# Performance work log

Hardware: AMD Instinct MI355X
Metric: run time of the kernel (lower is better)

Reference implementation:

```python
import jax, jax.numpy as jnp
import numpy as np

MASK_VALUE = -1e6  # torch code uses -1000000.0, not -inf


def setup_inputs() -> dict:
    key = jax.random.key(0)
    k1, k2, k3, k4 = jax.random.split(key, 4)
    B, Nq, Nk, d = 32, 2048, 2048, 128
    return {
        "querys": jax.random.normal(k1, (B, Nq, d), dtype=jnp.float32),
        "keys": jax.random.normal(k2, (B, Nk, d), dtype=jnp.float32),
        "values": jax.random.normal(k3, (B, Nk, d), dtype=jnp.float32),
        "valid_seq_len": jax.random.randint(k4, (B,), 1, Nk + 1, dtype=jnp.int32),
    }


def reference(querys, keys, values, valid_seq_len):
    # querys: [B, Nq, d], keys/values: [B, Nk, d], valid_seq_len: [B]
    d = querys.shape[-1]
    scale = 1.0 / jnp.sqrt(jnp.asarray(d, dtype=querys.dtype))
    # scores: [B, Nq, Nk]
    scores = jnp.einsum("bqd,bkd->bqk", querys, keys) * scale
    Nk = keys.shape[1]
    # mask key positions >= valid length (per batch, broadcast over queries)
    mask = jnp.arange(Nk, dtype=jnp.int32)[None, None, :] < valid_seq_len[:, None, None]
    scores = jnp.where(mask, scores, jnp.asarray(MASK_VALUE, dtype=scores.dtype))
    attn = jax.nn.softmax(scores, axis=-1)
    # dropout prob = 0.0 -> identity
    out = jnp.einsum("bqk,bkd->bqd", attn, values)
    return out
```

## Files before the change

kernel.cpp:

```cpp
#include <hip/hip_runtime.h>
#include <cstdint>
#include <math.h>

typedef unsigned short ushort_t;
typedef unsigned int uint_t;
typedef __bf16 v8bf __attribute__((ext_vector_type(8)));
typedef float v16f __attribute__((ext_vector_type(16)));

constexpr int B_SZ = 32, NQ = 2048, NK = 2048, DH = 128;
constexpr int BQ2 = 128, BK = 64;
constexpr int NQT = NQ / BQ2;
constexpr float QSCALE = 0.12751880226116815f;
constexpr float M2 = 17.312340490667561f;

__device__ inline int swzK(int row, int chunk) {
  return row * 128 + ((chunk ^ (row & 7)) << 3);
}
__device__ inline int swzV(int d, int chunk) {
  return d * 64 + ((chunk ^ (d & 7)) << 3);
}

__device__ __forceinline__ float4 ld4f(const float* p) {
  return *reinterpret_cast<const float4*>(p);
}
__device__ __forceinline__ uint4 ld4u(const ushort_t* p) {
  return *reinterpret_cast<const uint4*>(p);
}

__device__ inline v8bf cvt8(const float* __restrict__ p) {
  float4 f0 = ld4f(p);
  float4 f1 = ld4f(p + 4);
  v8bf r;
  r[0] = (__bf16)f0.x; r[1] = (__bf16)f0.y; r[2] = (__bf16)f0.z; r[3] = (__bf16)f0.w;
  r[4] = (__bf16)f1.x; r[5] = (__bf16)f1.y; r[6] = (__bf16)f1.z; r[7] = (__bf16)f1.w;
  return r;
}

__device__ inline v8bf cvt8s(const float* __restrict__ p, float s) {
  float4 f0 = ld4f(p);
  float4 f1 = ld4f(p + 4);
  v8bf r;
  r[0] = (__bf16)(f0.x * s); r[1] = (__bf16)(f0.y * s);
  r[2] = (__bf16)(f0.z * s); r[3] = (__bf16)(f0.w * s);
  r[4] = (__bf16)(f1.x * s); r[5] = (__bf16)(f1.y * s);
  r[6] = (__bf16)(f1.z * s); r[7] = (__bf16)(f1.w * s);
  return r;
}

__device__ inline v8bf cvt8r(const float4 f0, const float4 f1) {
  v8bf r;
  r[0] = (__bf16)f0.x; r[1] = (__bf16)f0.y; r[2] = (__bf16)f0.z; r[3] = (__bf16)f0.w;
  r[4] = (__bf16)f1.x; r[5] = (__bf16)f1.y; r[6] = (__bf16)f1.z; r[7] = (__bf16)f1.w;
  return r;
}

__device__ __forceinline__ uint_t pk2(float a, float b) {
  const ushort_t ua = __builtin_bit_cast(ushort_t, (__bf16)a);
  const ushort_t ub = __builtin_bit_cast(ushort_t, (__bf16)b);
  return (uint_t)ua | ((uint_t)ub << 16);
}

__global__ __launch_bounds__(256) void transpose_v(const float* __restrict__ V,
                                                   ushort_t* __restrict__ Vt) {
  __shared__ __align__(16) ushort_t st[64 * 128];
  const int b = blockIdx.y, k0 = blockIdx.x * 64, t = threadIdx.x;
  for (int c = 0; c < 4; ++c) {
    const int row = (t >> 4) + 16 * c;
    const int col = (t & 15) * 8;
    v8bf v = cvt8(V + ((size_t)(b * NK + k0 + row)) * DH + col);
    const int chunk = (col >> 3) ^ ((row >> 3) & 7);
    *reinterpret_cast<v8bf*>(&st[row * 128 + chunk * 8]) = v;
  }
  __syncthreads();
  for (int c = 0; c < 4; ++c) {
    const int d = (t >> 3) + 32 * c;
    const int kc = (t & 7) * 8;
    alignas(16) ushort_t tmp[8];
    for (int j = 0; j < 8; ++j) {
      const int row = kc + j;
      const int elem = (d & 7) | (((d >> 3) ^ ((row >> 3) & 7)) << 3);
      tmp[j] = st[row * 128 + elem];
    }
    *reinterpret_cast<uint4*>(Vt + ((size_t)(b * DH + d)) * NK + k0 + kc) =
        *reinterpret_cast<const uint4*>(tmp);
  }
}

__device__ __forceinline__ void qk_sm(const ushort_t* sk, int l32, int hi, int k0n,
                                      int valid, const v8bf* qf, float& ls0,
                                      float& ls1, uint4& pa0, uint4& pa1,
                                      uint4& pa2, uint4& pa3) {
  const bool part = (k0n + BK > valid);
#pragma unroll
  for (int kb = 0; kb < 2; ++kb) {
    const int rowA = kb * 32 + l32;
    const uint4 kf0 = ld4u(&sk[swzK(rowA, 0 + hi)]);
    const uint4 kf1 = ld4u(&sk[swzK(rowA, 2 + hi)]);
    const uint4 kf2 = ld4u(&sk[swzK(rowA, 4 + hi)]);
    const uint4 kf3 = ld4u(&sk[swzK(rowA, 6 + hi)]);
    const uint4 kf4 = ld4u(&sk[swzK(rowA, 8 + hi)]);
    const uint4 kf5 = ld4u(&sk[swzK(rowA, 10 + hi)]);
    const uint4 kf6 = ld4u(&sk[swzK(rowA, 12 + hi)]);
    const uint4 kf7 = ld4u(&sk[swzK(rowA, 14 + hi)]);
    v16f sa;
#pragma unroll
    for (int r = 0; r < 16; ++r) sa[r] = 0.f;
    __builtin_amdgcn_s_setprio(1);
    sa = __builtin_amdgcn_mfma_f32_32x32x16_bf16(__builtin_bit_cast(v8bf, kf0), qf[0], sa, 0, 0, 0);
    sa = __builtin_amdgcn_mfma_f32_32x32x16_bf16(__builtin_bit_cast(v8bf, kf1), qf[1], sa, 0, 0, 0);
    sa = __builtin_amdgcn_mfma_f32_32x32x16_bf16(__builtin_bit_cast(v8bf, kf2), qf[2], sa, 0, 0, 0);
    sa = __builtin_amdgcn_mfma_f32_32x32x16_bf16(__builtin_bit_cast(v8bf, kf3), qf[3], sa, 0, 0, 0);
    sa = __builtin_amdgcn_mfma_f32_32x32x16_bf16(__builtin_bit_cast(v8bf, kf4), qf[4], sa, 0, 0, 0);
    sa = __builtin_amdgcn_mfma_f32_32x32x16_bf16(__builtin_bit_cast(v8bf, kf5), qf[5], sa, 0, 0, 0);
    sa = __builtin_amdgcn_mfma_f32_32x32x16_bf16(__builtin_bit_cast(v8bf, kf6), qf[6], sa, 0, 0, 0);
    sa = __builtin_amdgcn_mfma_f32_32x32x16_bf16(__builtin_bit_cast(v8bf, kf7), qf[7], sa, 0, 0, 0);
    __builtin_amdgcn_s_setprio(0);
    float p[16];
#pragma unroll
    for (int r = 0; r < 16; ++r) {
      const int crow = (r & 3) + 8 * (r >> 2) + 4 * hi;
      float x = sa[r];
      if (part) x = (k0n + kb * 32 + crow < valid) ? x : -1e30f;
      float e;
      asm("v_exp_f32 %0, %1" : "=v"(e) : "v"(x - M2));
      p[r] = e;
      if (r < 8) ls0 += e; else ls1 += e;
    }
#pragma unroll
    for (int q2 = 0; q2 < 2; ++q2) {
      uint_t A0 = pk2(p[8 * q2 + 0], p[8 * q2 + 1]);
      uint_t A1 = pk2(p[8 * q2 + 2], p[8 * q2 + 3]);
      uint_t B0 = pk2(p[8 * q2 + 4], p[8 * q2 + 5]);
      uint_t B1 = pk2(p[8 * q2 + 6], p[8 * q2 + 7]);
      asm("v_permlane32_swap_b32 %0, %1" : "+v"(A0), "+v"(B0));
      asm("v_permlane32_swap_b32 %0, %1" : "+v"(A1), "+v"(B1));
      uint4 fw;
      fw.x = A0; fw.y = A1; fw.z = B0; fw.w = B1;
      if (kb == 0) { if (q2 == 0) pa0 = fw; else pa1 = fw; }
      else         { if (q2 == 0) pa2 = fw; else pa3 = fw; }
    }
  }
}

__device__ __forceinline__ void pv4(const ushort_t* sv, int l32, int hi,
                                    const uint4 paf, int ksg, v16f* o) {
  const uint4 vf0 = ld4u(&sv[swzV(0 + l32, 2 * ksg + hi)]);
  const uint4 vf1 = ld4u(&sv[swzV(32 + l32, 2 * ksg + hi)]);
  const uint4 vf2 = ld4u(&sv[swzV(64 + l32, 2 * ksg + hi)]);
  const uint4 vf3 = ld4u(&sv[swzV(96 + l32, 2 * ksg + hi)]);
  const v8bf pa = __builtin_bit_cast(v8bf, paf);
  __builtin_amdgcn_s_setprio(1);
  o[0] = __builtin_amdgcn_mfma_f32_32x32x16_bf16(pa, __builtin_bit_cast(v8bf, vf0), o[0], 0, 0, 0);
  o[1] = __builtin_amdgcn_mfma_f32_32x32x16_bf16(pa, __builtin_bit_cast(v8bf, vf1), o[1], 0, 0, 0);
  o[2] = __builtin_amdgcn_mfma_f32_32x32x16_bf16(pa, __builtin_bit_cast(v8bf, vf2), o[2], 0, 0, 0);
  o[3] = __builtin_amdgcn_mfma_f32_32x32x16_bf16(pa, __builtin_bit_cast(v8bf, vf3), o[3], 0, 0, 0);
  __builtin_amdgcn_s_setprio(0);
}

__global__ __launch_bounds__(256, 2) void attn(const float* __restrict__ Q,
                                               const float* __restrict__ K,
                                               const ushort_t* __restrict__ Vt,
                                               const int* __restrict__ vsl,
                                               float* __restrict__ Out) {
  __shared__ __align__(16) ushort_t sK2[2][64 * 128];
  __shared__ __align__(16) ushort_t sV2[2][DH * 64];

  const int t = threadIdx.x;
  const int lane = t & 63, w = t >> 6, hi = lane >> 5, l32 = lane & 31;

  int* s_ord = reinterpret_cast<int*>(sK2);
  if (t < 32) {
    const int cx = (vsl[t] + 63) >> 6;
    int rank = 0;
    for (int y = 0; y < 32; ++y) {
      const int cy = (vsl[y] + 63) >> 6;
      rank += (cy > cx) || (cy == cx && y < t);
    }
    s_ord[rank] = t;
  }
  __syncthreads();
  const int n = (int)blockIdx.x;
  const int ci = n & 255, cj = n >> 8;
  const int ru = cj ? 511 - ci : ci;
  const int b = s_ord[ru >> 4];
  const int qt2 = ru & 15;
  __syncthreads();

  const int q0 = qt2 * BQ2;
  const int valid = vsl[b];
  const int nt = (valid + BK - 1) / BK;

  v8bf qf[8];
  {
    const float* qp = Q + ((size_t)(b * NQ + q0 + w * 32 + l32)) * DH + hi * 8;
#pragma unroll
    for (int ks = 0; ks < 8; ++ks) qf[ks] = cvt8s(qp + ks * 16, QSCALE);
  }

  v16f o[4];
#pragma unroll
  for (int nb = 0; nb < 4; ++nb)
#pragma unroll
    for (int r = 0; r < 16; ++r) o[nb][r] = 0.f;
  float ls0 = 0.f, ls1 = 0.f;

  const float* Kb = K + (size_t)b * NK * DH;
  const ushort_t* Vb = Vt + (size_t)b * DH * NK;
  const int krow = t >> 4, kch = t & 15;
  const int vd = t >> 3, vch = t & 7;

  float4 k0a, k0b, k1a, k1b, k2a, k2b, k3a, k3b;
  uint4 v0r, v1r, v2r, v3r;

#define PREFETCH(KOFF)                                                   \
  do {                                                                   \
    const float* p0_ = Kb + (size_t)((KOFF) + krow) * DH + kch * 8;      \
    const float* p1_ = Kb + (size_t)((KOFF) + krow + 16) * DH + kch * 8; \
    const float* p2_ = Kb + (size_t)((KOFF) + krow + 32) * DH + kch * 8; \
    const float* p3_ = Kb + (size_t)((KOFF) + krow + 48) * DH + kch * 8; \
    k0a = ld4f(p0_); k0b = ld4f(p0_ + 4);                                \
    k1a = ld4f(p1_); k1b = ld4f(p1_ + 4);                                \
    k2a = ld4f(p2_); k2b = ld4f(p2_ + 4);                                \
    k3a = ld4f(p3_); k3b = ld4f(p3_ + 4);                                \
    const ushort_t* q0_ = Vb + (size_t)(vd)*NK + (KOFF) + vch * 8;       \
    const ushort_t* q1_ = Vb + (size_t)(vd + 32) * NK + (KOFF) + vch * 8;\
    const ushort_t* q2_ = Vb + (size_t)(vd + 64) * NK + (KOFF) + vch * 8;\
    const ushort_t* q3_ = Vb + (size_t)(vd + 96) * NK + (KOFF) + vch * 8;\
    v0r = ld4u(q0_); v1r = ld4u(q1_); v2r = ld4u(q2_); v3r = ld4u(q3_);  \
  } while (0)

#define STAGE(SK_, SV_)                                                      \
  do {                                                                       \
    *reinterpret_cast<v8bf*>(&(SK_)[swzK(krow + 0, kch)]) = cvt8r(k0a, k0b); \
    *reinterpret_cast<v8bf*>(&(SK_)[swzK(krow + 16, kch)]) = cvt8r(k1a, k1b);\
    *reinterpret_cast<v8bf*>(&(SK_)[swzK(krow + 32, kch)]) = cvt8r(k2a, k2b);\
    *reinterpret_cast<v8bf*>(&(SK_)[swzK(krow + 48, kch)]) = cvt8r(k3a, k3b);\
    *reinterpret_cast<uint4*>(&(SV_)[swzV(vd + 0, vch)]) = v0r;              \
    *reinterpret_cast<uint4*>(&(SV_)[swzV(vd + 32, vch)]) = v1r;             \
    *reinterpret_cast<uint4*>(&(SV_)[swzV(vd + 64, vch)]) = v2r;             \
    *reinterpret_cast<uint4*>(&(SV_)[swzV(vd + 96, vch)]) = v3r;             \
  } while (0)

  PREFETCH(0);
  STAGE(sK2[0], sV2[0]);
  if (nt > 1) PREFETCH(BK);
  __syncthreads();
  uint4 pa0, pa1, pa2, pa3;
  qk_sm(sK2[0], l32, hi, 0, valid, qf, ls0, ls1, pa0, pa1, pa2, pa3);

  for (int tile = 0; tile < nt; ++tile) {
    const int cur = tile & 1;
    if (tile + 1 < nt) {
      STAGE(sK2[cur ^ 1], sV2[cur ^ 1]);
      if (tile + 2 < nt) PREFETCH((tile + 2) * BK);
    }
    __syncthreads();
    pv4(sV2[cur], l32, hi, pa0, 0, o);
    pv4(sV2[cur], l32, hi, pa1, 1, o);
    pv4(sV2[cur], l32, hi, pa2, 2, o);
    pv4(sV2[cur], l32, hi, pa3, 3, o);
    if (tile + 1 < nt)
      qk_sm(sK2[cur ^ 1], l32, hi, (tile + 1) * BK, valid, qf, ls0, ls1, pa0, pa1,
            pa2, pa3);
    __syncthreads();
  }

  const float lsum = ls0 + ls1;
  const float rs = lsum + __shfl_xor(lsum, 32);
  const float inv_own = 1.0f / rs;
#pragma unroll
  for (int r = 0; r < 16; ++r) {
    const int crow = (r & 3) + 8 * (r >> 2) + 4 * hi;
    const float inv = __shfl(inv_own, crow);
    float* op = Out + ((size_t)(b * NQ + q0 + w * 32 + crow)) * DH + l32;
#pragma unroll
    for (int nb = 0; nb < 4; ++nb) op[nb * 32] = o[nb][r] * inv;
  }
#undef PREFETCH
#undef STAGE
}

extern "C" void kernel_launch(void* const* d_in, const int* in_sizes, int n_in,
                              void* d_out, int out_size, void* d_ws, size_t ws_size,
                              hipStream_t stream) {
  const float* Q = (const float*)d_in[0];
  const float* K = (const float*)d_in[1];
  const float* V = (const float*)d_in[2];
  const int* vsl = (const int*)d_in[3];
  float* Out = (float*)d_out;
  ushort_t* Vt = (ushort_t*)d_ws;

  transpose_v<<<dim3(NK / 64, B_SZ), dim3(256), 0, stream>>>(V, Vt);
  attn<<<dim3(B_SZ * NQT), dim3(256), 0, stream>>>(Q, K, Vt, vsl, Out);
}
```

Before: 198.2 us.

## Pre-pack K and V into MFMA fragment layout and split key tiles across wave pairs

After: 198.7 us. Within noise of the previous version (+0.3%).

```diff
diff --git a/kernel.cpp b/kernel.cpp
--- a/kernel.cpp
+++ b/kernel.cpp
@@ -8,17 +8,10 @@
 typedef float v16f __attribute__((ext_vector_type(16)));
 
 constexpr int B_SZ = 32, NQ = 2048, NK = 2048, DH = 128;
-constexpr int BQ2 = 128, BK = 64;
-constexpr int NQT = NQ / BQ2;
+constexpr int BK = 64;
+constexpr int TILE_E = 8192;
 constexpr float QSCALE = 0.12751880226116815f;
 constexpr float M2 = 17.312340490667561f;
-
-__device__ inline int swzK(int row, int chunk) {
-  return row * 128 + ((chunk ^ (row & 7)) << 3);
-}
-__device__ inline int swzV(int d, int chunk) {
-  return d * 64 + ((chunk ^ (d & 7)) << 3);
-}
 
 __device__ __forceinline__ float4 ld4f(const float* p) {
   return *reinterpret_cast<const float4*>(p);
@@ -47,23 +40,30 @@
   return r;
 }
 
-__device__ inline v8bf cvt8r(const float4 f0, const float4 f1) {
-  v8bf r;
-  r[0] = (__bf16)f0.x; r[1] = (__bf16)f0.y; r[2] = (__bf16)f0.z; r[3] = (__bf16)f0.w;
-  r[4] = (__bf16)f1.x; r[5] = (__bf16)f1.y; r[6] = (__bf16)f1.z; r[7] = (__bf16)f1.w;
-  return r;
-}
-
 __device__ __forceinline__ uint_t pk2(float a, float b) {
   const ushort_t ua = __builtin_bit_cast(ushort_t, (__bf16)a);
   const ushort_t ub = __builtin_bit_cast(ushort_t, (__bf16)b);
   return (uint_t)ua | ((uint_t)ub << 16);
 }
 
-__global__ __launch_bounds__(256) void transpose_v(const float* __restrict__ V,
-                                                   ushort_t* __restrict__ Vt) {
+__global__ __launch_bounds__(256) void prep_k(const float* __restrict__ K,
+                                              ushort_t* __restrict__ Kf) {
+  const int b = blockIdx.y, tq = blockIdx.x, t = threadIdx.x;
+  const int l32 = t & 31, g = t >> 5;
+  const float* Kb = K + ((size_t)(b * NK + tq * 64)) * DH;
+  ushort_t* out = Kf + ((size_t)(b * 32 + tq)) * TILE_E;
+  for (int c = 0; c < 4; ++c) {
+    const int id = g * 4 + c;
+    const int kb = id >> 4, ks = (id >> 1) & 7, hi = id & 1;
+    v8bf v = cvt8(Kb + (size_t)(kb * 32 + l32) * DH + (2 * ks + hi) * 8);
+    *reinterpret_cast<v8bf*>(out + (size_t)id * 256 + l32 * 8) = v;
+  }
+}
+
+__global__ __launch_bounds__(256) void prep_v(const float* __restrict__ V,
+                                              ushort_t* __restrict__ Vf) {
   __shared__ __align__(16) ushort_t st[64 * 128];
-  const int b = blockIdx.y, k0 = blockIdx.x * 64, t = threadIdx.x;
+  const int b = blockIdx.y, tq = blockIdx.x, k0 = tq * 64, t = threadIdx.x;
   for (int c = 0; c < 4; ++c) {
     const int row = (t >> 4) + 16 * c;
     const int col = (t & 15) * 8;
@@ -72,36 +72,39 @@
     *reinterpret_cast<v8bf*>(&st[row * 128 + chunk * 8]) = v;
   }
   __syncthreads();
+  ushort_t* out = Vf + ((size_t)(b * 32 + tq)) * TILE_E;
+  const int l32 = t & 31, f0 = t >> 5;
   for (int c = 0; c < 4; ++c) {
-    const int d = (t >> 3) + 32 * c;
-    const int kc = (t & 7) * 8;
+    const int f = f0 + 8 * c;
+    const int nb = f & 3, hi = (f >> 2) & 1, ksg = f >> 3;
+    const int d = nb * 32 + l32;
     alignas(16) ushort_t tmp[8];
     for (int j = 0; j < 8; ++j) {
-      const int row = kc + j;
+      const int row = ksg * 16 + hi * 8 + j;
       const int elem = (d & 7) | (((d >> 3) ^ ((row >> 3) & 7)) << 3);
       tmp[j] = st[row * 128 + elem];
     }
-    *reinterpret_cast<uint4*>(Vt + ((size_t)(b * DH + d)) * NK + k0 + kc) =
+    *reinterpret_cast<uint4*>(out + ((ksg * 2 + hi) * 4 + nb) * 256 + l32 * 8) =
         *reinterpret_cast<const uint4*>(tmp);
   }
 }
 
-__device__ __forceinline__ void qk_sm(const ushort_t* sk, int l32, int hi, int k0n,
+__device__ __forceinline__ void qk_sm(const ushort_t* kt, int l32, int hi, int k0n,
                                       int valid, const v8bf* qf, float& ls0,
                                       float& ls1, uint4& pa0, uint4& pa1,
                                       uint4& pa2, uint4& pa3) {
   const bool part = (k0n + BK > valid);
 #pragma unroll
   for (int kb = 0; kb < 2; ++kb) {
-    const int rowA = kb * 32 + l32;
-    const uint4 kf0 = ld4u(&sk[swzK(rowA, 0 + hi)]);
-    const uint4 kf1 = ld4u(&sk[swzK(rowA, 2 + hi)]);
-    const uint4 kf2 = ld4u(&sk[swzK(rowA, 4 + hi)]);
-    const uint4 kf3 = ld4u(&sk[swzK(rowA, 6 + hi)]);
-    const uint4 kf4 = ld4u(&sk[swzK(rowA, 8 + hi)]);
-    const uint4 kf5 = ld4u(&sk[swzK(rowA, 10 + hi)]);
-    const uint4 kf6 = ld4u(&sk[swzK(rowA, 12 + hi)]);
-    const uint4 kf7 = ld4u(&sk[swzK(rowA, 14 + hi)]);
+    const ushort_t* base = kt + kb * 4096 + hi * 256 + l32 * 8;
+    const uint4 kf0 = ld4u(base + 0 * 512);
+    const uint4 kf1 = ld4u(base + 1 * 512);
+    const uint4 kf2 = ld4u(base + 2 * 512);
+    const uint4 kf3 = ld4u(base + 3 * 512);
+    const uint4 kf4 = ld4u(base + 4 * 512);
+    const uint4 kf5 = ld4u(base + 5 * 512);
+    const uint4 kf6 = ld4u(base + 6 * 512);
+    const uint4 kf7 = ld4u(base + 7 * 512);
     v16f sa;
 #pragma unroll
     for (int r = 0; r < 16; ++r) sa[r] = 0.f;
@@ -142,12 +145,13 @@
   }
 }
 
-__device__ __forceinline__ void pv4(const ushort_t* sv, int l32, int hi,
+__device__ __forceinline__ void pv4(const ushort_t* vt, int l32, int hi,
                                     const uint4 paf, int ksg, v16f* o) {
-  const uint4 vf0 = ld4u(&sv[swzV(0 + l32, 2 * ksg + hi)]);
-  const uint4 vf1 = ld4u(&sv[swzV(32 + l32, 2 * ksg + hi)]);
-  const uint4 vf2 = ld4u(&sv[swzV(64 + l32, 2 * ksg + hi)]);
-  const uint4 vf3 = ld4u(&sv[swzV(96 + l32, 2 * ksg + hi)]);
+  const ushort_t* vb = vt + ksg * 2048 + hi * 1024 + l32 * 8;
+  const uint4 vf0 = ld4u(vb + 0 * 256);
+  const uint4 vf1 = ld4u(vb + 1 * 256);
+  const uint4 vf2 = ld4u(vb + 2 * 256);
+  const uint4 vf3 = ld4u(vb + 3 * 256);
   const v8bf pa = __builtin_bit_cast(v8bf, paf);
   __builtin_amdgcn_s_setprio(1);
   o[0] = __builtin_amdgcn_mfma_f32_32x32x16_bf16(pa, __builtin_bit_cast(v8bf, vf0), o[0], 0, 0, 0);
@@ -158,17 +162,19 @@
 }
 
 __global__ __launch_bounds__(256, 2) void attn(const float* __restrict__ Q,
-                                               const float* __restrict__ K,
-                                               const ushort_t* __restrict__ Vt,
+                                               const ushort_t* __restrict__ Kf,
+                                               const ushort_t* __restrict__ Vf,
                                                const int* __restrict__ vsl,
                                                float* __restrict__ Out) {
-  __shared__ __align__(16) ushort_t sK2[2][64 * 128];
-  __shared__ __align__(16) ushort_t sV2[2][DH * 64];
+  __shared__ int s_ord[32];
+  __shared__ float mO[2][4096];
+  __shared__ float sRS[2][32];
 
   const int t = threadIdx.x;
-  const int lane = t & 63, w = t >> 6, hi = lane >> 5, l32 = lane & 31;
-
-  int* s_ord = reinterpret_cast<int*>(sK2);
+  const int lane = t & 63, w = t >> 6;
+  const int wq = w & 1, pr = w >> 1;
+  const int hi = lane >> 5, l32 = lane & 31;
+
   if (t < 32) {
     const int cx = (vsl[t] + 63) >> 6;
     int rank = 0;
@@ -181,18 +187,18 @@
   __syncthreads();
   const int n = (int)blockIdx.x;
   const int ci = n & 255, cj = n >> 8;
-  const int ru = cj ? 511 - ci : ci;
-  const int b = s_ord[ru >> 4];
-  const int qt2 = ru & 15;
-  __syncthreads();
-
-  const int q0 = qt2 * BQ2;
+  const int rk = (cj == 0) ? ci : (cj == 1) ? 511 - ci : (cj == 2) ? 512 + ci : 1023 - ci;
+  const int b = s_ord[rk >> 5];
+  const int qt = rk & 31;
+
+  const int q0 = qt * 64;
   const int valid = vsl[b];
   const int nt = (valid + BK - 1) / BK;
+  const int myNt = (nt + 1 - pr) >> 1;
 
   v8bf qf[8];
   {
-    const float* qp = Q + ((size_t)(b * NQ + q0 + w * 32 + l32)) * DH + hi * 8;
+    const float* qp = Q + ((size_t)(b * NQ + q0 + wq * 32 + l32)) * DH + hi * 8;
 #pragma unroll
     for (int ks = 0; ks < 8; ++ks) qf[ks] = cvt8s(qp + ks * 16, QSCALE);
   }
@@ -204,80 +210,48 @@
     for (int r = 0; r < 16; ++r) o[nb][r] = 0.f;
   float ls0 = 0.f, ls1 = 0.f;
 
-  const float* Kb = K + (size_t)b * NK * DH;
-  const ushort_t* Vb = Vt + (size_t)b * DH * NK;
-  const int krow = t >> 4, kch = t & 15;
-  const int vd = t >> 3, vch = t & 7;
-
-  float4 k0a, k0b, k1a, k1b, k2a, k2b, k3a, k3b;
-  uint4 v0r, v1r, v2r, v3r;
-
-#define PREFETCH(KOFF)                                                   \
-  do {                                                                   \
-    const float* p0_ = Kb + (size_t)((KOFF) + krow) * DH + kch * 8;      \
-    const float* p1_ = Kb + (size_t)((KOFF) + krow + 16) * DH + kch * 8; \
-    const float* p2_ = Kb + (size_t)((KOFF) + krow + 32) * DH + kch * 8; \
-    const float* p3_ = Kb + (size_t)((KOFF) + krow + 48) * DH + kch * 8; \
-    k0a = ld4f(p0_); k0b = ld4f(p0_ + 4);                                \
-    k1a = ld4f(p1_); k1b = ld4f(p1_ + 4);                                \
-    k2a = ld4f(p2_); k2b = ld4f(p2_ + 4);                                \
-    k3a = ld4f(p3_); k3b = ld4f(p3_ + 4);                                \
-    const ushort_t* q0_ = Vb + (size_t)(vd)*NK + (KOFF) + vch * 8;       \
-    const ushort_t* q1_ = Vb + (size_t)(vd + 32) * NK + (KOFF) + vch * 8;\
-    const ushort_t* q2_ = Vb + (size_t)(vd + 64) * NK + (KOFF) + vch * 8;\
-    const ushort_t* q3_ = Vb + (size_t)(vd + 96) * NK + (KOFF) + vch * 8;\
-    v0r = ld4u(q0_); v1r = ld4u(q1_); v2r = ld4u(q2_); v3r = ld4u(q3_);  \
-  } while (0)
-
-#define STAGE(SK_, SV_)                                                      \
-  do {                                                                       \
-    *reinterpret_cast<v8bf*>(&(SK_)[swzK(krow + 0, kch)]) = cvt8r(k0a, k0b); \
-    *reinterpret_cast<v8bf*>(&(SK_)[swzK(krow + 16, kch)]) = cvt8r(k1a, k1b);\
-    *reinterpret_cast<v8bf*>(&(SK_)[swzK(krow + 32, kch)]) = cvt8r(k2a, k2b);\
-    *reinterpret_cast<v8bf*>(&(SK_)[swzK(krow + 48, kch)]) = cvt8r(k3a, k3b);\
-    *reinterpret_cast<uint4*>(&(SV_)[swzV(vd + 0, vch)]) = v0r;              \
-    *reinterpret_cast<uint4*>(&(SV_)[swzV(vd + 32, vch)]) = v1r;             \
-    *reinterpret_cast<uint4*>(&(SV_)[swzV(vd + 64, vch)]) = v2r;             \
-    *reinterpret_cast<uint4*>(&(SV_)[swzV(vd + 96, vch)]) = v3r;             \
-  } while (0)
-
-  PREFETCH(0);
-  STAGE(sK2[0], sV2[0]);
-  if (nt > 1) PREFETCH(BK);
+  const ushort_t* Kb = Kf + (size_t)b * 32 * TILE_E;
+  const ushort_t* Vb = Vf + (size_t)b * 32 * TILE_E;
+
+  for (int i = 0; i < myNt; ++i) {
+    const int tile = 2 * i + pr;
+    const ushort_t* kt = Kb + (size_t)tile * TILE_E;
+    const ushort_t* vt = Vb + (size_t)tile * TILE_E;
+    uint4 pa0, pa1, pa2, pa3;
+    qk_sm(kt, l32, hi, tile * BK, valid, qf, ls0, ls1, pa0, pa1, pa2, pa3);
+    pv4(vt, l32, hi, pa0, 0, o);
+    pv4(vt, l32, hi, pa1, 1, o);
+    pv4(vt, l32, hi, pa2, 2, o);
+    pv4(vt, l32, hi, pa3, 3, o);
+  }
+
+  const float lsw = ls0 + ls1;
+  const float rsw = lsw + __shfl_xor(lsw, 32);
+  if (pr == 1) {
+#pragma unroll
+    for (int nb = 0; nb < 4; ++nb)
+#pragma unroll
+      for (int r = 0; r < 16; ++r)
+        mO[wq][(nb * 16 + r) * 64 + lane] = o[nb][r];
+    if (hi == 0) sRS[wq][l32] = rsw;
+  }
   __syncthreads();
-  uint4 pa0, pa1, pa2, pa3;
-  qk_sm(sK2[0], l32, hi, 0, valid, qf, ls0, ls1, pa0, pa1, pa2, pa3);
-
-  for (int tile = 0; tile < nt; ++tile) {
-    const int cur = tile & 1;
-    if (tile + 1 < nt) {
-      STAGE(sK2[cur ^ 1], sV2[cur ^ 1]);
-      if (tile + 2 < nt) PREFETCH((tile + 2) * BK);
-    }
-    __syncthreads();
-    pv4(sV2[cur], l32, hi, pa0, 0, o);
-    pv4(sV2[cur], l32, hi, pa1, 1, o);
-    pv4(sV2[cur], l32, hi, pa2, 2, o);
-    pv4(sV2[cur], l32, hi, pa3, 3, o);
-    if (tile + 1 < nt)
-      qk_sm(sK2[cur ^ 1], l32, hi, (tile + 1) * BK, valid, qf, ls0, ls1, pa0, pa1,
-            pa2, pa3);
-    __syncthreads();
-  }
-
-  const float lsum = ls0 + ls1;
-  const float rs = lsum + __shfl_xor(lsum, 32);
-  const float inv_own = 1.0f / rs;
-#pragma unroll
-  for (int r = 0; r < 16; ++r) {
-    const int crow = (r & 3) + 8 * (r >> 2) + 4 * hi;
-    const float inv = __shfl(inv_own, crow);
-    float* op = Out + ((size_t)(b * NQ + q0 + w * 32 + crow)) * DH + l32;
-#pragma unroll
-    for (int nb = 0; nb < 4; ++nb) op[nb * 32] = o[nb][r] * inv;
-  }
-#undef PREFETCH
-#undef STAGE
+  if (pr == 0) {
+    const float rs = rsw + sRS[wq][l32];
+#pragma unroll
+    for (int nb = 0; nb < 4; ++nb)
+#pragma unroll
+      for (int r = 0; r < 16; ++r) o[nb][r] += mO[wq][(nb * 16 + r) * 64 + lane];
+    const float inv_own = 1.0f / rs;
+#pragma unroll
+    for (int r = 0; r < 16; ++r) {
+      const int crow = (r & 3) + 8 * (r >> 2) + 4 * hi;
+      const float inv = __shfl(inv_own, crow);
+      float* op = Out + ((size_t)(b * NQ + q0 + wq * 32 + crow)) * DH + l32;
+#pragma unroll
+      for (int nb = 0; nb < 4; ++nb) op[nb * 32] = o[nb][r] * inv;
+    }
+  }
 }
 
 extern "C" void kernel_launch(void* const* d_in, const int* in_sizes, int n_in,
@@ -288,8 +262,11 @@
   const float* V = (const float*)d_in[2];
   const int* vsl = (const int*)d_in[3];
   float* Out = (float*)d_out;
-  ushort_t* Vt = (ushort_t*)d_ws;
-
-  transpose_v<<<dim3(NK / 64, B_SZ), dim3(256), 0, stream>>>(V, Vt);
-  attn<<<dim3(B_SZ * NQT), dim3(256), 0, stream>>>(Q, K, Vt, vsl, Out);
-}
+
+  ushort_t* Kf = (ushort_t*)d_ws;
+  ushort_t* Vf = Kf + (size_t)B_SZ * 32 * TILE_E;
+
+  prep_k<<<dim3(NK / 64, B_SZ), dim3(256), 0, stream>>>(K, Kf);
+  prep_v<<<dim3(NK / 64, B_SZ), dim3(256), 0, stream>>>(V, Vf);
+  attn<<<dim3(1024), dim3(256), 0, stream>>>(Q, Kf, Vf, vsl, Out);
+}
```
